# Kernel optimization log

Measured on AMD Instinct MI355X. Metric: run time of the kernel, lower is better.

The kernel has to match this reference:

```python
import jax, jax.numpy as jnp
import numpy as np

H = 8              # n_heads
N_PER_GRAPH = 64   # nodes per graph (equal-sized graphs)


def setup_inputs() -> dict:
    key = jax.random.key(0)
    ks = jax.random.split(key, 5)
    total, D = 65536, 512
    x = jax.random.normal(ks[0], (total, D), dtype=jnp.float32)
    batch = jnp.arange(total, dtype=jnp.int64) // N_PER_GRAPH  # sorted graph ids
    s = 1.0 / np.sqrt(D).astype(np.float32)
    # nn.MultiheadAttention packed in-proj (xavier-ish uniform) + zero bias
    in_proj_w = jax.random.uniform(ks[1], (3 * D, D), jnp.float32, -s, s)
    in_proj_b = jnp.zeros((3 * D,), jnp.float32)
    out_proj_w = jax.random.uniform(ks[2], (D, D), jnp.float32, -s, s)
    out_proj_b = jnp.zeros((D,), jnp.float32)
    gate_w = jax.random.uniform(ks[3], (1, D), jnp.float32, -s, s)
    gate_b = jnp.zeros((1,), jnp.float32)
    return {"x": x, "batch": batch, "in_proj_w": in_proj_w, "in_proj_b": in_proj_b,
            "out_proj_w": out_proj_w, "out_proj_b": out_proj_b,
            "gate_w": gate_w, "gate_b": gate_b}


def reference(x, batch, in_proj_w, in_proj_b, out_proj_w, out_proj_b, gate_w, gate_b):
    total, D = x.shape
    G = total // N_PER_GRAPH
    hd = D // H
    xg = x.reshape(G, N_PER_GRAPH, D)                       # [G, N, D]
    # packed qkv projection (torch: x @ in_proj_w.T + in_proj_b)
    qkv = jnp.einsum('gnd,ed->gne', xg, in_proj_w) + in_proj_b
    q, k, v = jnp.split(qkv, 3, axis=-1)
    def to_heads(t):
        return t.reshape(G, N_PER_GRAPH, H, hd).transpose(0, 2, 1, 3)  # [G, H, N, hd]
    q, k, v = to_heads(q), to_heads(k), to_heads(v)
    scores = jnp.einsum('ghnd,ghmd->ghnm', q, k) * (1.0 / np.sqrt(hd))
    attn = jax.nn.softmax(scores, axis=-1)
    ctx = jnp.einsum('ghnm,ghmd->ghnd', attn, v)
    ctx = ctx.transpose(0, 2, 1, 3).reshape(G, N_PER_GRAPH, D)
    attn_out = jnp.einsum('gnd,ed->gne', ctx, out_proj_w) + out_proj_b  # [G, N, D]
    gates = jax.nn.sigmoid(jnp.einsum('gnd,od->gno', attn_out, gate_w) + gate_b)
    return (attn_out * gates).sum(axis=1)                   # [G, D]
```

## Files before the change

kernel.cpp:

```cpp
#include <hip/hip_runtime.h>
#include <stdint.h>


typedef __attribute__((ext_vector_type(8))) short short8;
typedef __attribute__((ext_vector_type(4))) float f32x4;

#define D_ 512

#define WQKV_OFF   0u
#define WO_OFF     1572864u
#define UPART_OFF  2097152u
#define SG_OFF     2132032u
#define WCTX_OFF   2136128u
#define SCR_OFF    3184704u

__device__ __forceinline__ unsigned short f2bf(float f) {
    union { float f; unsigned int u; } t; t.f = f;
    unsigned int u = t.u;
    return (unsigned short)((u + 0x7FFFu + ((u >> 16) & 1u)) >> 16);
}
__device__ __forceinline__ unsigned pack2(float a, float b) {
    return (unsigned)f2bf(a) | ((unsigned)f2bf(b) << 16);
}

__global__ __launch_bounds__(256)
void convert_weights(const float* __restrict__ wqkv, const float* __restrict__ wo,
                     unsigned short* __restrict__ wbf,
                     const float* __restrict__ gw, float* __restrict__ upart) {
    if (blockIdx.x >= 1024) {
        const int b = blockIdx.x - 1024;
        const int t = threadIdx.x;
        float a0 = 0.f, a1 = 0.f;
        #pragma unroll 4
        for (int e = b * 32; e < b * 32 + 32; ++e) {
            const float ge = gw[e];
            a0 += wo[(size_t)e * 512 + t]       * ge;
            a1 += wo[(size_t)e * 512 + t + 256] * ge;
        }
        upart[b * 512 + t] = a0; upart[b * 512 + t + 256] = a1;
        return;
    }
    const int i4 = blockIdx.x * 256 + threadIdx.x;
    float4 v;
    if (i4 < 196608) v = *(const float4*)(wqkv + (size_t)i4 * 4);
    else             v = *(const float4*)(wo   + (size_t)(i4 - 196608) * 4);
    uint2 p; p.x = pack2(v.x, v.y); p.y = pack2(v.z, v.w);
    *(uint2*)(wbf + (size_t)i4 * 4) = p;
}

union U8 { unsigned u[4]; short8 s; };

__global__ __launch_bounds__(512, 2)
void attn_ctx_gscr(const float* __restrict__ x,
                   const unsigned short* __restrict__ wqkv,
                   const float* __restrict__ bqkv,
                   const float* __restrict__ upart,
                   const float* __restrict__ bo,
                   const float* __restrict__ gw,
                   const float* __restrict__ gb,
                   unsigned short* __restrict__ scr_g,
                   unsigned short* __restrict__ wctx_ws,
                   float* __restrict__ sumgate)
{
    __shared__ unsigned short xs[64][520];
    __shared__ float logitp[8][64];
    __shared__ float gatev[64];
    __shared__ float u_s[512];
    __shared__ float c0_s;

    const int g    = blockIdx.x;
    const int tid  = threadIdx.x;
    const int w    = tid >> 6;
    const int lane = tid & 63;
    const int l15  = lane & 15;
    const int quad = lane >> 4;

    #pragma unroll
    for (int i = 0; i < 16; ++i) {
        int idx = tid + i * 512;
        int row = idx >> 7;
        int c4  = idx & 127;
        float4 v = *(const float4*)(x + ((size_t)(g*64 + row))*512 + c4*4);
        uint2 p; p.x = pack2(v.x, v.y); p.y = pack2(v.z, v.w);
        *(uint2*)(&xs[row][c4*4]) = p;
    }
    {
        float s = 0.f;
        #pragma unroll
        for (int b = 0; b < 16; ++b) s += upart[b*512 + tid];
        u_s[tid] = s;
    }
    if (tid < 64) {
        float s = 0.f;
        #pragma unroll
        for (int i = 0; i < 8; ++i) s += bo[tid*8 + i] * gw[tid*8 + i];
        s += __shfl_xor(s, 1);  s += __shfl_xor(s, 2);  s += __shfl_xor(s, 4);
        s += __shfl_xor(s, 8);  s += __shfl_xor(s, 16); s += __shfl_xor(s, 32);
        if (tid == 0) c0_s = s + gb[0];
    }
    __syncthreads();

    const int h = w;
    unsigned short* Sg = scr_g + ((size_t)(g*8 + w) << 12);

    U8 qA[4][2], kB[4][2];
    #pragma unroll
    for (int dt = 0; dt < 4; ++dt) {
        f32x4 aq[4], ak[4], av[4];
        #pragma unroll
        for (int nt = 0; nt < 4; ++nt) {
            aq[nt] = (f32x4){0.f,0.f,0.f,0.f};
            ak[nt] = (f32x4){0.f,0.f,0.f,0.f};
            av[nt] = (f32x4){0.f,0.f,0.f,0.f};
        }
        const unsigned short* wq = wqkv + (size_t)(          h*64 + dt*16 + l15) * 512;
        const unsigned short* wk = wqkv + (size_t)( 512 +    h*64 + dt*16 + l15) * 512;
        const unsigned short* wv = wqkv + (size_t)(1024 +    h*64 + dt*16 + l15) * 512;
        #pragma unroll 4
        for (int ks = 0; ks < 16; ++ks) {
            const int col = ks*32 + quad*8;
            short8 a0 = *(const short8*)(wq + col);
            short8 a1 = *(const short8*)(wk + col);
            short8 a2 = *(const short8*)(wv + col);
            #pragma unroll
            for (int nt = 0; nt < 4; ++nt) {
                short8 b = *(const short8*)(&xs[nt*16 + l15][col]);
                aq[nt] = __builtin_amdgcn_mfma_f32_16x16x32_bf16(a0, b, aq[nt], 0,0,0);
                ak[nt] = __builtin_amdgcn_mfma_f32_16x16x32_bf16(a1, b, ak[nt], 0,0,0);
                av[nt] = __builtin_amdgcn_mfma_f32_16x16x32_bf16(a2, b, av[nt], 0,0,0);
            }
        }
        float bq[4], bk2[4], bv2[4];
        #pragma unroll
        for (int r = 0; r < 4; ++r) {
            bq[r]  = bqkv[          h*64 + dt*16 + quad*4 + r];
            bk2[r] = bqkv[ 512 +    h*64 + dt*16 + quad*4 + r];
            bv2[r] = bqkv[1024 +    h*64 + dt*16 + quad*4 + r];
        }
        const bool take = ((quad >> 1) == (dt & 1));
        const int  ks2  = dt >> 1;
        #pragma unroll
        for (int nt = 0; nt < 4; ++nt) {
            unsigned q01 = pack2(aq[nt][0]+bq[0],  aq[nt][1]+bq[1]);
            unsigned q23 = pack2(aq[nt][2]+bq[2],  aq[nt][3]+bq[3]);
            unsigned k01 = pack2(ak[nt][0]+bk2[0], ak[nt][1]+bk2[1]);
            unsigned k23 = pack2(ak[nt][2]+bk2[2], ak[nt][3]+bk2[3]);
            #pragma unroll
            for (int j = 0; j < 4; ++j) {
                int srcl = ((quad & 1)*2 + (j >> 1))*16 + l15;
                unsigned tq = (unsigned)__shfl((int)((j & 1) ? q23 : q01), srcl);
                unsigned tk = (unsigned)__shfl((int)((j & 1) ? k23 : k01), srcl);
                if (take) { qA[nt][ks2].u[j] = tq; kB[nt][ks2].u[j] = tk; }
            }
            #pragma unroll
            for (int r = 0; r < 4; ++r)
                Sg[(dt*16 + quad*4 + r)*64 + nt*16 + l15] = f2bf(av[nt][r] + bv2[r]);
        }
    }

    f32x4 sacc[4][4];
    #pragma unroll
    for (int a = 0; a < 4; ++a)
        #pragma unroll
        for (int b = 0; b < 4; ++b) sacc[a][b] = (f32x4){0.f,0.f,0.f,0.f};
    #pragma unroll
    for (int ks2 = 0; ks2 < 2; ++ks2)
        #pragma unroll
        for (int a = 0; a < 4; ++a)
            #pragma unroll
            for (int b = 0; b < 4; ++b)
                sacc[a][b] = __builtin_amdgcn_mfma_f32_16x16x32_bf16(
                                 qA[a][ks2].s, kB[b][ks2].s, sacc[a][b], 0,0,0);

    #pragma unroll
    for (int a = 0; a < 4; ++a) {
        #pragma unroll
        for (int r = 0; r < 4; ++r) {
            float m0 = -1e30f;
            #pragma unroll
            for (int b = 0; b < 4; ++b) { sacc[a][b][r] *= 0.125f; m0 = fmaxf(m0, sacc[a][b][r]); }
            m0 = fmaxf(m0, __shfl_xor(m0, 1));
            m0 = fmaxf(m0, __shfl_xor(m0, 2));
            m0 = fmaxf(m0, __shfl_xor(m0, 4));
            m0 = fmaxf(m0, __shfl_xor(m0, 8));
            float s = 0.f;
            #pragma unroll
            for (int b = 0; b < 4; ++b) { float e = __expf(sacc[a][b][r] - m0); sacc[a][b][r] = e; s += e; }
            s += __shfl_xor(s, 1); s += __shfl_xor(s, 2); s += __shfl_xor(s, 4); s += __shfl_xor(s, 8);
            float inv = 1.0f / s;
            #pragma unroll
            for (int b = 0; b < 4; ++b) sacc[a][b][r] *= inv;
        }
    }

    U8 vA[4][2];
    #pragma unroll
    for (int dtile = 0; dtile < 4; ++dtile)
        #pragma unroll
        for (int ks2 = 0; ks2 < 2; ++ks2)
            vA[dtile][ks2].s = *(const short8*)(Sg + (dtile*16 + l15)*64 + ks2*32 + quad*8);
    asm volatile("s_waitcnt vmcnt(0)" ::: "memory");

    #pragma unroll
    for (int a = 0; a < 4; ++a)
        #pragma unroll
        for (int b = 0; b < 4; ++b)
            #pragma unroll
            for (int r = 0; r < 4; ++r)
                Sg[(a*16 + quad*4 + r)*64 + b*16 + l15] = f2bf(sacc[a][b][r]);
    asm volatile("s_waitcnt vmcnt(0)" ::: "memory");

    U8 pB[4][2];
    #pragma unroll
    for (int a = 0; a < 4; ++a)
        #pragma unroll
        for (int ks2 = 0; ks2 < 2; ++ks2)
            pB[a][ks2].s = *(const short8*)(Sg + (a*16 + l15)*64 + ks2*32 + quad*8);

    f32x4 cacc[4][4];
    #pragma unroll
    for (int dtile = 0; dtile < 4; ++dtile)
        #pragma unroll
        for (int a = 0; a < 4; ++a) cacc[dtile][a] = (f32x4){0.f,0.f,0.f,0.f};
    #pragma unroll
    for (int ks2 = 0; ks2 < 2; ++ks2)
        #pragma unroll
        for (int dtile = 0; dtile < 4; ++dtile)
            #pragma unroll
            for (int a = 0; a < 4; ++a)
                cacc[dtile][a] = __builtin_amdgcn_mfma_f32_16x16x32_bf16(
                                     vA[dtile][ks2].s, pB[a][ks2].s, cacc[dtile][a], 0,0,0);

    {
        float uv[4][4];
        #pragma unroll
        for (int dtile = 0; dtile < 4; ++dtile)
            #pragma unroll
            for (int r = 0; r < 4; ++r)
                uv[dtile][r] = u_s[h*64 + dtile*16 + quad*4 + r];
        #pragma unroll
        for (int a = 0; a < 4; ++a) {
            float s = 0.f;
            #pragma unroll
            for (int dtile = 0; dtile < 4; ++dtile)
                #pragma unroll
                for (int r = 0; r < 4; ++r)
                    s += cacc[dtile][a][r] * uv[dtile][r];
            s += __shfl_xor(s, 16); s += __shfl_xor(s, 32);
            if (quad == 0) logitp[w][a*16 + l15] = s;
        }
    }
    __syncthreads();

    if (tid < 64) {
        float lg = c0_s;
        #pragma unroll
        for (int ww = 0; ww < 8; ++ww) lg += logitp[ww][tid];
        float gt = 1.0f / (1.0f + __expf(-lg));
        gatev[tid] = gt;
        float s = gt;
        s += __shfl_xor(s, 1);  s += __shfl_xor(s, 2);  s += __shfl_xor(s, 4);
        s += __shfl_xor(s, 8);  s += __shfl_xor(s, 16); s += __shfl_xor(s, 32);
        if (tid == 0) sumgate[g] = s;
    }
    __syncthreads();

    {
        float gv[4];
        #pragma unroll
        for (int a = 0; a < 4; ++a) gv[a] = gatev[a*16 + l15];
        #pragma unroll
        for (int dtile = 0; dtile < 4; ++dtile) {
            float sr[4];
            #pragma unroll
            for (int r = 0; r < 4; ++r) {
                float s = cacc[dtile][0][r]*gv[0] + cacc[dtile][1][r]*gv[1]
                        + cacc[dtile][2][r]*gv[2] + cacc[dtile][3][r]*gv[3];
                s += __shfl_xor(s, 1); s += __shfl_xor(s, 2);
                s += __shfl_xor(s, 4); s += __shfl_xor(s, 8);
                sr[r] = s;
            }
            if (l15 == 0) {
                uint2 pk; pk.x = pack2(sr[0], sr[1]); pk.y = pack2(sr[2], sr[3]);
                *(uint2*)(wctx_ws + (size_t)g*512 + h*64 + dtile*16 + quad*4) = pk;
            }
        }
    }
}

__global__ __launch_bounds__(512, 2)
void attn_ctx_lds(const float* __restrict__ x,
                  const unsigned short* __restrict__ wqkv,
                  const float* __restrict__ bqkv,
                  const float* __restrict__ upart,
                  const float* __restrict__ bo,
                  const float* __restrict__ gw,
                  const float* __restrict__ gb,
                  unsigned short* __restrict__ wctx_ws,
                  float* __restrict__ sumgate)
{
    __shared__ unsigned short xs[64][520];
    __shared__ unsigned short scr[8][64][72];
    __shared__ float logitp[8][64];
    __shared__ float gatev[64];
    __shared__ float u_s[512];
    __shared__ float c0_s;

    const int g    = blockIdx.x;
    const int tid  = threadIdx.x;
    const int w    = tid >> 6;
    const int lane = tid & 63;
    const int l15  = lane & 15;
    const int quad = lane >> 4;

    #pragma unroll
    for (int i = 0; i < 16; ++i) {
        int idx = tid + i * 512;
        int row = idx >> 7;
        int c4  = idx & 127;
        float4 v = *(const float4*)(x + ((size_t)(g*64 + row))*512 + c4*4);
        uint2 p; p.x = pack2(v.x, v.y); p.y = pack2(v.z, v.w);
        *(uint2*)(&xs[row][c4*4]) = p;
    }
    {
        float s = 0.f;
        #pragma unroll
        for (int b = 0; b < 16; ++b) s += upart[b*512 + tid];
        u_s[tid] = s;
    }
    if (tid < 64) {
        float s = 0.f;
        #pragma unroll
        for (int i = 0; i < 8; ++i) s += bo[tid*8 + i] * gw[tid*8 + i];
        s += __shfl_xor(s, 1);  s += __shfl_xor(s, 2);  s += __shfl_xor(s, 4);
        s += __shfl_xor(s, 8);  s += __shfl_xor(s, 16); s += __shfl_xor(s, 32);
        if (tid == 0) c0_s = s + gb[0];
    }
    __syncthreads();

    const int h = w;
    unsigned short (*S)[72] = scr[w];

    U8 qA[4][2], kB[4][2];
    #pragma unroll
    for (int dt = 0; dt < 4; ++dt) {
        f32x4 aq[4], ak[4], av[4];
        #pragma unroll
        for (int nt = 0; nt < 4; ++nt) {
            aq[nt] = (f32x4){0.f,0.f,0.f,0.f};
            ak[nt] = (f32x4){0.f,0.f,0.f,0.f};
            av[nt] = (f32x4){0.f,0.f,0.f,0.f};
        }
        const unsigned short* wq = wqkv + (size_t)(          h*64 + dt*16 + l15) * 512;
        const unsigned short* wk = wqkv + (size_t)( 512 +    h*64 + dt*16 + l15) * 512;
        const unsigned short* wv = wqkv + (size_t)(1024 +    h*64 + dt*16 + l15) * 512;
        #pragma unroll 4
        for (int ks = 0; ks < 16; ++ks) {
            const int col = ks*32 + quad*8;
            short8 a0 = *(const short8*)(wq + col);
            short8 a1 = *(const short8*)(wk + col);
            short8 a2 = *(const short8*)(wv + col);
            #pragma unroll
            for (int nt = 0; nt < 4; ++nt) {
                short8 b = *(const short8*)(&xs[nt*16 + l15][col]);
                aq[nt] = __builtin_amdgcn_mfma_f32_16x16x32_bf16(a0, b, aq[nt], 0,0,0);
                ak[nt] = __builtin_amdgcn_mfma_f32_16x16x32_bf16(a1, b, ak[nt], 0,0,0);
                av[nt] = __builtin_amdgcn_mfma_f32_16x16x32_bf16(a2, b, av[nt], 0,0,0);
            }
        }
        float bq[4], bk2[4], bv2[4];
        #pragma unroll
        for (int r = 0; r < 4; ++r) {
            bq[r]  = bqkv[          h*64 + dt*16 + quad*4 + r];
            bk2[r] = bqkv[ 512 +    h*64 + dt*16 + quad*4 + r];
            bv2[r] = bqkv[1024 +    h*64 + dt*16 + quad*4 + r];
        }
        const bool take = ((quad >> 1) == (dt & 1));
        const int  ks2  = dt >> 1;
        #pragma unroll
        for (int nt = 0; nt < 4; ++nt) {
            unsigned q01 = pack2(aq[nt][0]+bq[0],  aq[nt][1]+bq[1]);
            unsigned q23 = pack2(aq[nt][2]+bq[2],  aq[nt][3]+bq[3]);
            unsigned k01 = pack2(ak[nt][0]+bk2[0], ak[nt][1]+bk2[1]);
            unsigned k23 = pack2(ak[nt][2]+bk2[2], ak[nt][3]+bk2[3]);
            #pragma unroll
            for (int j = 0; j < 4; ++j) {
                int srcl = ((quad & 1)*2 + (j >> 1))*16 + l15;
                unsigned tq = (unsigned)__shfl((int)((j & 1) ? q23 : q01), srcl);
                unsigned tk = (unsigned)__shfl((int)((j & 1) ? k23 : k01), srcl);
                if (take) { qA[nt][ks2].u[j] = tq; kB[nt][ks2].u[j] = tk; }
            }
            #pragma unroll
            for (int r = 0; r < 4; ++r)
                S[dt*16 + quad*4 + r][nt*16 + l15] = f2bf(av[nt][r] + bv2[r]);
        }
    }

    f32x4 sacc[4][4];
    #pragma unroll
    for (int a = 0; a < 4; ++a)
        #pragma unroll
        for (int b = 0; b < 4; ++b) sacc[a][b] = (f32x4){0.f,0.f,0.f,0.f};
    #pragma unroll
    for (int ks2 = 0; ks2 < 2; ++ks2)
        #pragma unroll
        for (int a = 0; a < 4; ++a)
            #pragma unroll
            for (int b = 0; b < 4; ++b)
                sacc[a][b] = __builtin_amdgcn_mfma_f32_16x16x32_bf16(
                                 qA[a][ks2].s, kB[b][ks2].s, sacc[a][b], 0,0,0);

    #pragma unroll
    for (int a = 0; a < 4; ++a) {
        #pragma unroll
        for (int r = 0; r < 4; ++r) {
            float m0 = -1e30f;
            #pragma unroll
            for (int b = 0; b < 4; ++b) { sacc[a][b][r] *= 0.125f; m0 = fmaxf(m0, sacc[a][b][r]); }
            m0 = fmaxf(m0, __shfl_xor(m0, 1));
            m0 = fmaxf(m0, __shfl_xor(m0, 2));
            m0 = fmaxf(m0, __shfl_xor(m0, 4));
            m0 = fmaxf(m0, __shfl_xor(m0, 8));
            float s = 0.f;
            #pragma unroll
            for (int b = 0; b < 4; ++b) { float e = __expf(sacc[a][b][r] - m0); sacc[a][b][r] = e; s += e; }
            s += __shfl_xor(s, 1); s += __shfl_xor(s, 2); s += __shfl_xor(s, 4); s += __shfl_xor(s, 8);
            float inv = 1.0f / s;
            #pragma unroll
            for (int b = 0; b < 4; ++b) sacc[a][b][r] *= inv;
        }
    }

    U8 vA[4][2];
    #pragma unroll
    for (int dtile = 0; dtile < 4; ++dtile)
        #pragma unroll
        for (int ks2 = 0; ks2 < 2; ++ks2)
            vA[dtile][ks2].s = *(const short8*)(&S[dtile*16 + l15][ks2*32 + quad*8]);

    #pragma unroll
    for (int a = 0; a < 4; ++a)
        #pragma unroll
        for (int b = 0; b < 4; ++b)
            #pragma unroll
            for (int r = 0; r < 4; ++r)
                S[a*16 + quad*4 + r][b*16 + l15] = f2bf(sacc[a][b][r]);

    U8 pB[4][2];
    #pragma unroll
    for (int a = 0; a < 4; ++a)
        #pragma unroll
        for (int ks2 = 0; ks2 < 2; ++ks2)
            pB[a][ks2].s = *(const short8*)(&S[a*16 + l15][ks2*32 + quad*8]);

    f32x4 cacc[4][4];
    #pragma unroll
    for (int dtile = 0; dtile < 4; ++dtile)
        #pragma unroll
        for (int a = 0; a < 4; ++a) cacc[dtile][a] = (f32x4){0.f,0.f,0.f,0.f};
    #pragma unroll
    for (int ks2 = 0; ks2 < 2; ++ks2)
        #pragma unroll
        for (int dtile = 0; dtile < 4; ++dtile)
            #pragma unroll
            for (int a = 0; a < 4; ++a)
                cacc[dtile][a] = __builtin_amdgcn_mfma_f32_16x16x32_bf16(
                                     vA[dtile][ks2].s, pB[a][ks2].s, cacc[dtile][a], 0,0,0);

    {
        float uv[4][4];
        #pragma unroll
        for (int dtile = 0; dtile < 4; ++dtile)
            #pragma unroll
            for (int r = 0; r < 4; ++r)
                uv[dtile][r] = u_s[h*64 + dtile*16 + quad*4 + r];
        #pragma unroll
        for (int a = 0; a < 4; ++a) {
            float s = 0.f;
            #pragma unroll
            for (int dtile = 0; dtile < 4; ++dtile)
                #pragma unroll
                for (int r = 0; r < 4; ++r)
                    s += cacc[dtile][a][r] * uv[dtile][r];
            s += __shfl_xor(s, 16); s += __shfl_xor(s, 32);
            if (quad == 0) logitp[w][a*16 + l15] = s;
        }
    }
    __syncthreads();

    if (tid < 64) {
        float lg = c0_s;
        #pragma unroll
        for (int ww = 0; ww < 8; ++ww) lg += logitp[ww][tid];
        float gt = 1.0f / (1.0f + __expf(-lg));
        gatev[tid] = gt;
        float s = gt;
        s += __shfl_xor(s, 1);  s += __shfl_xor(s, 2);  s += __shfl_xor(s, 4);
        s += __shfl_xor(s, 8);  s += __shfl_xor(s, 16); s += __shfl_xor(s, 32);
        if (tid == 0) sumgate[g] = s;
    }
    __syncthreads();

    {
        float gv[4];
        #pragma unroll
        for (int a = 0; a < 4; ++a) gv[a] = gatev[a*16 + l15];
        #pragma unroll
        for (int dtile = 0; dtile < 4; ++dtile) {
            float sr[4];
            #pragma unroll
            for (int r = 0; r < 4; ++r) {
                float s = cacc[dtile][0][r]*gv[0] + cacc[dtile][1][r]*gv[1]
                        + cacc[dtile][2][r]*gv[2] + cacc[dtile][3][r]*gv[3];
                s += __shfl_xor(s, 1); s += __shfl_xor(s, 2);
                s += __shfl_xor(s, 4); s += __shfl_xor(s, 8);
                sr[r] = s;
            }
            if (l15 == 0) {
                uint2 pk; pk.x = pack2(sr[0], sr[1]); pk.y = pack2(sr[2], sr[3]);
                *(uint2*)(wctx_ws + (size_t)g*512 + h*64 + dtile*16 + quad*4) = pk;
            }
        }
    }
}

__global__ __launch_bounds__(256, 4)
void outproj_kernel(const unsigned short* __restrict__ wo_bf,
                    const unsigned short* __restrict__ wctx_bf,
                    const float* __restrict__ bo,
                    const float* __restrict__ sumgate,
                    float* __restrict__ out)
{
    const int tid  = threadIdx.x;
    const int w    = tid >> 6;
    const int lane = tid & 63;
    const int l15  = lane & 15;
    const int quad = lane >> 4;
    const int g0   = blockIdx.x * 16;
    const int e0   = blockIdx.y * 64;

    f32x4 oac = (f32x4){0.f,0.f,0.f,0.f};
    #pragma unroll 4
    for (int ks = 0; ks < 16; ++ks) {
        const int col = ks*32 + quad*8;
        short8 a = *(const short8*)(wctx_bf + (size_t)(g0 + l15)*D_ + col);
        short8 b = *(const short8*)(wo_bf + (size_t)(e0 + w*16 + l15)*D_ + col);
        oac = __builtin_amdgcn_mfma_f32_16x16x32_bf16(a, b, oac, 0,0,0);
    }
    const int e = e0 + w*16 + l15;
    const float bov = bo[e];
    #pragma unroll
    for (int r = 0; r < 4; ++r) {
        const int gg = g0 + quad*4 + r;
        out[(size_t)gg*D_ + e] = oac[r] + sumgate[gg] * bov;
    }
}

extern "C" void kernel_launch(void* const* d_in, const int* in_sizes, int n_in,
                              void* d_out, int out_size, void* d_ws, size_t ws_size,
                              hipStream_t stream) {
    const float* x    = (const float*)d_in[0];
    const float* wqkv = (const float*)d_in[2];
    const float* bqkv = (const float*)d_in[3];
    const float* wo   = (const float*)d_in[4];
    const float* bo   = (const float*)d_in[5];
    const float* gw   = (const float*)d_in[6];
    const float* gb   = (const float*)d_in[7];
    float* out = (float*)d_out;

    char* ws = (char*)d_ws;
    unsigned short* wqkv_bf = (unsigned short*)(ws + WQKV_OFF);
    unsigned short* wo_bf   = (unsigned short*)(ws + WO_OFF);
    float*          upart   = (float*)(ws + UPART_OFF);
    float*          sg_ws   = (float*)(ws + SG_OFF);
    unsigned short* wctx_ws = (unsigned short*)(ws + WCTX_OFF);
    unsigned short* scr_g   = (unsigned short*)(ws + SCR_OFF);

    const int total = in_sizes[0] / D_;
    const int G     = total / 64;

    const size_t need_fast = (size_t)SCR_OFF + (size_t)G * 8 * 8192;
    const bool   fast      = ws_size >= need_fast;

    hipLaunchKernelGGL(convert_weights, dim3(1040), dim3(256), 0, stream,
                       wqkv, wo, wqkv_bf, gw, upart);
    if (fast) {
        hipLaunchKernelGGL(attn_ctx_gscr, dim3(G), dim3(512), 0, stream,
                           x, wqkv_bf, bqkv, upart, bo, gw, gb, scr_g, wctx_ws, sg_ws);
    } else {
        hipLaunchKernelGGL(attn_ctx_lds, dim3(G), dim3(512), 0, stream,
                           x, wqkv_bf, bqkv, upart, bo, gw, gb, wctx_ws, sg_ws);
    }
    hipLaunchKernelGGL(outproj_kernel, dim3(G/16, 8), dim3(256), 0, stream,
                       wo_bf, wctx_ws, bo, sg_ws, out);
}
```

Before: 434.6 us.

## Fuse weight conversion, attention, and out-projection into one cooperative persistent kernel

Replaces the three-kernel pipeline with a single cooperative kernel of 256 persistent blocks. Grid-wide syncs separate three phases: weight conversion to bf16, per-graph attention with a loop over graphs, and the output projection. The global-memory scratch path for V and P is dropped in favour of LDS scratch. The aim is to remove launch gaps and global scratch traffic. In exchange, only 256 blocks run with low occupancy, work per block is serialized, and a launch fallback is kept.

```diff
diff --git a/kernel.cpp b/kernel.cpp
--- a/kernel.cpp
+++ b/kernel.cpp
@@ -1,6 +1,9 @@
 #include <hip/hip_runtime.h>
+#include <hip/hip_cooperative_groups.h>
 #include <stdint.h>
 
+
+namespace cg = cooperative_groups;
 
 typedef __attribute__((ext_vector_type(8))) short short8;
 typedef __attribute__((ext_vector_type(4))) float f32x4;
@@ -12,7 +15,6 @@
 #define UPART_OFF  2097152u
 #define SG_OFF     2132032u
 #define WCTX_OFF   2136128u
-#define SCR_OFF    3184704u
 
 __device__ __forceinline__ unsigned short f2bf(float f) {
     union { float f; unsigned int u; } t; t.f = f;
@@ -21,6 +23,296 @@
 }
 __device__ __forceinline__ unsigned pack2(float a, float b) {
     return (unsigned)f2bf(a) | ((unsigned)f2bf(b) << 16);
+}
+
+union U8 { unsigned u[4]; short8 s; };
+
+__global__ __launch_bounds__(512, 2)
+void fused_all(const float* __restrict__ x,
+               const float* __restrict__ wqkv_f,
+               const float* __restrict__ wo_f,
+               const float* __restrict__ bqkv,
+               const float* __restrict__ bo,
+               const float* __restrict__ gw,
+               const float* __restrict__ gb,
+               unsigned short* __restrict__ wbf,
+               float* __restrict__ upart,
+               unsigned short* __restrict__ wctx_ws,
+               float* __restrict__ sumgate,
+               float* __restrict__ out,
+               int G)
+{
+    __shared__ unsigned short xs[64][520];
+    __shared__ unsigned short scr[8][64][72];
+    __shared__ float logitp[8][64];
+    __shared__ float gatev[64];
+    __shared__ float u_s[512];
+    __shared__ float c0_s;
+
+    const int bid  = blockIdx.x;
+    const int tid  = threadIdx.x;
+    const int w    = tid >> 6;
+    const int lane = tid & 63;
+    const int l15  = lane & 15;
+    const int quad = lane >> 4;
+
+    for (int i4 = bid * 512 + tid; i4 < 262144; i4 += 256 * 512) {
+        float4 v;
+        if (i4 < 196608) v = *(const float4*)(wqkv_f + (size_t)i4 * 4);
+        else             v = *(const float4*)(wo_f   + (size_t)(i4 - 196608) * 4);
+        uint2 p; p.x = pack2(v.x, v.y); p.y = pack2(v.z, v.w);
+        *(uint2*)(wbf + (size_t)i4 * 4) = p;
+    }
+    if (bid < 16) {
+        float a = 0.f;
+        #pragma unroll 4
+        for (int e = bid * 32; e < bid * 32 + 32; ++e)
+            a += wo_f[(size_t)e * 512 + tid] * gw[e];
+        upart[bid * 512 + tid] = a;
+    }
+    cg::this_grid().sync();
+
+    const unsigned short* wqkv  = wbf;
+    const unsigned short* wo_bf = wbf + 786432;
+
+    {
+        float s = 0.f;
+        #pragma unroll
+        for (int b = 0; b < 16; ++b) s += upart[b*512 + tid];
+        u_s[tid] = s;
+    }
+    if (tid < 64) {
+        float s = 0.f;
+        #pragma unroll
+        for (int i = 0; i < 8; ++i) s += bo[tid*8 + i] * gw[tid*8 + i];
+        s += __shfl_xor(s, 1);  s += __shfl_xor(s, 2);  s += __shfl_xor(s, 4);
+        s += __shfl_xor(s, 8);  s += __shfl_xor(s, 16); s += __shfl_xor(s, 32);
+        if (tid == 0) c0_s = s + gb[0];
+    }
+    __syncthreads();
+
+    const int h = w;
+    unsigned short (*S)[72] = scr[w];
+
+    for (int g = bid; g < G; g += 256) {
+        #pragma unroll
+        for (int i = 0; i < 16; ++i) {
+            int idx = tid + i * 512;
+            int row = idx >> 7;
+            int c4  = idx & 127;
+            float4 v = *(const float4*)(x + ((size_t)(g*64 + row))*512 + c4*4);
+            uint2 p; p.x = pack2(v.x, v.y); p.y = pack2(v.z, v.w);
+            *(uint2*)(&xs[row][c4*4]) = p;
+        }
+        __syncthreads();
+
+        U8 qA[4][2], kB[4][2];
+        #pragma unroll
+        for (int dt = 0; dt < 4; ++dt) {
+            f32x4 aq[4], ak[4], av[4];
+            #pragma unroll
+            for (int nt = 0; nt < 4; ++nt) {
+                aq[nt] = (f32x4){0.f,0.f,0.f,0.f};
+                ak[nt] = (f32x4){0.f,0.f,0.f,0.f};
+                av[nt] = (f32x4){0.f,0.f,0.f,0.f};
+            }
+            const unsigned short* wq = wqkv + (size_t)(          h*64 + dt*16 + l15) * 512;
+            const unsigned short* wk = wqkv + (size_t)( 512 +    h*64 + dt*16 + l15) * 512;
+            const unsigned short* wv = wqkv + (size_t)(1024 +    h*64 + dt*16 + l15) * 512;
+            #pragma unroll 4
+            for (int ks = 0; ks < 16; ++ks) {
+                const int col = ks*32 + quad*8;
+                short8 a0 = *(const short8*)(wq + col);
+                short8 a1 = *(const short8*)(wk + col);
+                short8 a2 = *(const short8*)(wv + col);
+                #pragma unroll
+                for (int nt = 0; nt < 4; ++nt) {
+                    short8 b = *(const short8*)(&xs[nt*16 + l15][col]);
+                    aq[nt] = __builtin_amdgcn_mfma_f32_16x16x32_bf16(a0, b, aq[nt], 0,0,0);
+                    ak[nt] = __builtin_amdgcn_mfma_f32_16x16x32_bf16(a1, b, ak[nt], 0,0,0);
+                    av[nt] = __builtin_amdgcn_mfma_f32_16x16x32_bf16(a2, b, av[nt], 0,0,0);
+                }
+            }
+            float bq[4], bk2[4], bv2[4];
+            #pragma unroll
+            for (int r = 0; r < 4; ++r) {
+                bq[r]  = bqkv[          h*64 + dt*16 + quad*4 + r];
+                bk2[r] = bqkv[ 512 +    h*64 + dt*16 + quad*4 + r];
+                bv2[r] = bqkv[1024 +    h*64 + dt*16 + quad*4 + r];
+            }
+            const bool take = ((quad >> 1) == (dt & 1));
+            const int  ks2  = dt >> 1;
+            #pragma unroll
+            for (int nt = 0; nt < 4; ++nt) {
+                unsigned q01 = pack2(aq[nt][0]+bq[0],  aq[nt][1]+bq[1]);
+                unsigned q23 = pack2(aq[nt][2]+bq[2],  aq[nt][3]+bq[3]);
+                unsigned k01 = pack2(ak[nt][0]+bk2[0], ak[nt][1]+bk2[1]);
+                unsigned k23 = pack2(ak[nt][2]+bk2[2], ak[nt][3]+bk2[3]);
+                #pragma unroll
+                for (int j = 0; j < 4; ++j) {
+                    int srcl = ((quad & 1)*2 + (j >> 1))*16 + l15;
+                    unsigned tq = (unsigned)__shfl((int)((j & 1) ? q23 : q01), srcl);
+                    unsigned tk = (unsigned)__shfl((int)((j & 1) ? k23 : k01), srcl);
+                    if (take) { qA[nt][ks2].u[j] = tq; kB[nt][ks2].u[j] = tk; }
+                }
+                #pragma unroll
+                for (int r = 0; r < 4; ++r)
+                    S[dt*16 + quad*4 + r][nt*16 + l15] = f2bf(av[nt][r] + bv2[r]);
+            }
+        }
+
+        f32x4 sacc[4][4];
+        #pragma unroll
+        for (int a = 0; a < 4; ++a)
+            #pragma unroll
+            for (int b = 0; b < 4; ++b) sacc[a][b] = (f32x4){0.f,0.f,0.f,0.f};
+        #pragma unroll
+        for (int ks2 = 0; ks2 < 2; ++ks2)
+            #pragma unroll
+            for (int a = 0; a < 4; ++a)
+                #pragma unroll
+                for (int b = 0; b < 4; ++b)
+                    sacc[a][b] = __builtin_amdgcn_mfma_f32_16x16x32_bf16(
+                                     qA[a][ks2].s, kB[b][ks2].s, sacc[a][b], 0,0,0);
+
+        #pragma unroll
+        for (int a = 0; a < 4; ++a) {
+            #pragma unroll
+            for (int r = 0; r < 4; ++r) {
+                float m0 = -1e30f;
+                #pragma unroll
+                for (int b = 0; b < 4; ++b) { sacc[a][b][r] *= 0.125f; m0 = fmaxf(m0, sacc[a][b][r]); }
+                m0 = fmaxf(m0, __shfl_xor(m0, 1));
+                m0 = fmaxf(m0, __shfl_xor(m0, 2));
+                m0 = fmaxf(m0, __shfl_xor(m0, 4));
+                m0 = fmaxf(m0, __shfl_xor(m0, 8));
+                float s = 0.f;
+                #pragma unroll
+                for (int b = 0; b < 4; ++b) { float e = __expf(sacc[a][b][r] - m0); sacc[a][b][r] = e; s += e; }
+                s += __shfl_xor(s, 1); s += __shfl_xor(s, 2); s += __shfl_xor(s, 4); s += __shfl_xor(s, 8);
+                float inv = 1.0f / s;
+                #pragma unroll
+                for (int b = 0; b < 4; ++b) sacc[a][b][r] *= inv;
+            }
+        }
+
+        U8 vA[4][2];
+        #pragma unroll
+        for (int dtile = 0; dtile < 4; ++dtile)
+            #pragma unroll
+            for (int ks2 = 0; ks2 < 2; ++ks2)
+                vA[dtile][ks2].s = *(const short8*)(&S[dtile*16 + l15][ks2*32 + quad*8]);
+
+        #pragma unroll
+        for (int a = 0; a < 4; ++a)
+            #pragma unroll
+            for (int b = 0; b < 4; ++b)
+                #pragma unroll
+                for (int r = 0; r < 4; ++r)
+                    S[a*16 + quad*4 + r][b*16 + l15] = f2bf(sacc[a][b][r]);
+
+        U8 pB[4][2];
+        #pragma unroll
+        for (int a = 0; a < 4; ++a)
+            #pragma unroll
+            for (int ks2 = 0; ks2 < 2; ++ks2)
+                pB[a][ks2].s = *(const short8*)(&S[a*16 + l15][ks2*32 + quad*8]);
+
+        f32x4 cacc[4][4];
+        #pragma unroll
+        for (int dtile = 0; dtile < 4; ++dtile)
+            #pragma unroll
+            for (int a = 0; a < 4; ++a) cacc[dtile][a] = (f32x4){0.f,0.f,0.f,0.f};
+        #pragma unroll
+        for (int ks2 = 0; ks2 < 2; ++ks2)
+            #pragma unroll
+            for (int dtile = 0; dtile < 4; ++dtile)
+                #pragma unroll
+                for (int a = 0; a < 4; ++a)
+                    cacc[dtile][a] = __builtin_amdgcn_mfma_f32_16x16x32_bf16(
+                                         vA[dtile][ks2].s, pB[a][ks2].s, cacc[dtile][a], 0,0,0);
+
+        {
+            float uv[4][4];
+            #pragma unroll
+            for (int dtile = 0; dtile < 4; ++dtile)
+                #pragma unroll
+                for (int r = 0; r < 4; ++r)
+                    uv[dtile][r] = u_s[h*64 + dtile*16 + quad*4 + r];
+            #pragma unroll
+            for (int a = 0; a < 4; ++a) {
+                float s = 0.f;
+                #pragma unroll
+                for (int dtile = 0; dtile < 4; ++dtile)
+                    #pragma unroll
+                    for (int r = 0; r < 4; ++r)
+                        s += cacc[dtile][a][r] * uv[dtile][r];
+                s += __shfl_xor(s, 16); s += __shfl_xor(s, 32);
+                if (quad == 0) logitp[w][a*16 + l15] = s;
+            }
+        }
+        __syncthreads();
+
+        if (tid < 64) {
+            float lg = c0_s;
+            #pragma unroll
+            for (int ww = 0; ww < 8; ++ww) lg += logitp[ww][tid];
+            float gt = 1.0f / (1.0f + __expf(-lg));
+            gatev[tid] = gt;
+            float s = gt;
+            s += __shfl_xor(s, 1);  s += __shfl_xor(s, 2);  s += __shfl_xor(s, 4);
+            s += __shfl_xor(s, 8);  s += __shfl_xor(s, 16); s += __shfl_xor(s, 32);
+            if (tid == 0) sumgate[g] = s;
+        }
+        __syncthreads();
+
+        {
+            float gv[4];
+            #pragma unroll
+            for (int a = 0; a < 4; ++a) gv[a] = gatev[a*16 + l15];
+            #pragma unroll
+            for (int dtile = 0; dtile < 4; ++dtile) {
+                float sr[4];
+                #pragma unroll
+                for (int r = 0; r < 4; ++r) {
+                    float s = cacc[dtile][0][r]*gv[0] + cacc[dtile][1][r]*gv[1]
+                            + cacc[dtile][2][r]*gv[2] + cacc[dtile][3][r]*gv[3];
+                    s += __shfl_xor(s, 1); s += __shfl_xor(s, 2);
+                    s += __shfl_xor(s, 4); s += __shfl_xor(s, 8);
+                    sr[r] = s;
+                }
+                if (l15 == 0) {
+                    uint2 pk; pk.x = pack2(sr[0], sr[1]); pk.y = pack2(sr[2], sr[3]);
+                    *(uint2*)(wctx_ws + (size_t)g*512 + h*64 + dtile*16 + quad*4) = pk;
+                }
+            }
+        }
+        __syncthreads();
+    }
+
+    cg::this_grid().sync();
+
+    const int GX = G >> 4;
+    for (int job = bid; job < GX * 4; job += 256) {
+        const int gx = job % GX;
+        const int e0 = (job / GX) * 128;
+        const int g0 = gx * 16;
+        f32x4 oac = (f32x4){0.f,0.f,0.f,0.f};
+        #pragma unroll 4
+        for (int ks = 0; ks < 16; ++ks) {
+            const int col = ks*32 + quad*8;
+            short8 a = *(const short8*)(wctx_ws + (size_t)(g0 + l15)*D_ + col);
+            short8 b = *(const short8*)(wo_bf + (size_t)(e0 + w*16 + l15)*D_ + col);
+            oac = __builtin_amdgcn_mfma_f32_16x16x32_bf16(a, b, oac, 0,0,0);
+        }
+        const int e = e0 + w*16 + l15;
+        const float bov = bo[e];
+        #pragma unroll
+        for (int r = 0; r < 4; ++r) {
+            const int gg = g0 + quad*4 + r;
+            out[(size_t)gg*D_ + e] = oac[r] + sumgate[gg] * bov;
+        }
+    }
 }
 
 __global__ __launch_bounds__(256)
@@ -48,256 +340,16 @@
     *(uint2*)(wbf + (size_t)i4 * 4) = p;
 }
 
-union U8 { unsigned u[4]; short8 s; };
-
 __global__ __launch_bounds__(512, 2)
-void attn_ctx_gscr(const float* __restrict__ x,
-                   const unsigned short* __restrict__ wqkv,
-                   const float* __restrict__ bqkv,
-                   const float* __restrict__ upart,
-                   const float* __restrict__ bo,
-                   const float* __restrict__ gw,
-                   const float* __restrict__ gb,
-                   unsigned short* __restrict__ scr_g,
-                   unsigned short* __restrict__ wctx_ws,
-                   float* __restrict__ sumgate)
-{
-    __shared__ unsigned short xs[64][520];
-    __shared__ float logitp[8][64];
-    __shared__ float gatev[64];
-    __shared__ float u_s[512];
-    __shared__ float c0_s;
-
-    const int g    = blockIdx.x;
-    const int tid  = threadIdx.x;
-    const int w    = tid >> 6;
-    const int lane = tid & 63;
-    const int l15  = lane & 15;
-    const int quad = lane >> 4;
-
-    #pragma unroll
-    for (int i = 0; i < 16; ++i) {
-        int idx = tid + i * 512;
-        int row = idx >> 7;
-        int c4  = idx & 127;
-        float4 v = *(const float4*)(x + ((size_t)(g*64 + row))*512 + c4*4);
-        uint2 p; p.x = pack2(v.x, v.y); p.y = pack2(v.z, v.w);
-        *(uint2*)(&xs[row][c4*4]) = p;
-    }
-    {
-        float s = 0.f;
-        #pragma unroll
-        for (int b = 0; b < 16; ++b) s += upart[b*512 + tid];
-        u_s[tid] = s;
-    }
-    if (tid < 64) {
-        float s = 0.f;
-        #pragma unroll
-        for (int i = 0; i < 8; ++i) s += bo[tid*8 + i] * gw[tid*8 + i];
-        s += __shfl_xor(s, 1);  s += __shfl_xor(s, 2);  s += __shfl_xor(s, 4);
-        s += __shfl_xor(s, 8);  s += __shfl_xor(s, 16); s += __shfl_xor(s, 32);
-        if (tid == 0) c0_s = s + gb[0];
-    }
-    __syncthreads();
-
-    const int h = w;
-    unsigned short* Sg = scr_g + ((size_t)(g*8 + w) << 12);
-
-    U8 qA[4][2], kB[4][2];
-    #pragma unroll
-    for (int dt = 0; dt < 4; ++dt) {
-        f32x4 aq[4], ak[4], av[4];
-        #pragma unroll
-        for (int nt = 0; nt < 4; ++nt) {
-            aq[nt] = (f32x4){0.f,0.f,0.f,0.f};
-            ak[nt] = (f32x4){0.f,0.f,0.f,0.f};
-            av[nt] = (f32x4){0.f,0.f,0.f,0.f};
-        }
-        const unsigned short* wq = wqkv + (size_t)(          h*64 + dt*16 + l15) * 512;
-        const unsigned short* wk = wqkv + (size_t)( 512 +    h*64 + dt*16 + l15) * 512;
-        const unsigned short* wv = wqkv + (size_t)(1024 +    h*64 + dt*16 + l15) * 512;
-        #pragma unroll 4
-        for (int ks = 0; ks < 16; ++ks) {
-            const int col = ks*32 + quad*8;
-            short8 a0 = *(const short8*)(wq + col);
-            short8 a1 = *(const short8*)(wk + col);
-            short8 a2 = *(const short8*)(wv + col);
-            #pragma unroll
-            for (int nt = 0; nt < 4; ++nt) {
-                short8 b = *(const short8*)(&xs[nt*16 + l15][col]);
-                aq[nt] = __builtin_amdgcn_mfma_f32_16x16x32_bf16(a0, b, aq[nt], 0,0,0);
-                ak[nt] = __builtin_amdgcn_mfma_f32_16x16x32_bf16(a1, b, ak[nt], 0,0,0);
-                av[nt] = __builtin_amdgcn_mfma_f32_16x16x32_bf16(a2, b, av[nt], 0,0,0);
-            }
-        }
-        float bq[4], bk2[4], bv2[4];
-        #pragma unroll
-        for (int r = 0; r < 4; ++r) {
-            bq[r]  = bqkv[          h*64 + dt*16 + quad*4 + r];
-            bk2[r] = bqkv[ 512 +    h*64 + dt*16 + quad*4 + r];
-            bv2[r] = bqkv[1024 +    h*64 + dt*16 + quad*4 + r];
-        }
-        const bool take = ((quad >> 1) == (dt & 1));
-        const int  ks2  = dt >> 1;
-        #pragma unroll
-        for (int nt = 0; nt < 4; ++nt) {
-            unsigned q01 = pack2(aq[nt][0]+bq[0],  aq[nt][1]+bq[1]);
-            unsigned q23 = pack2(aq[nt][2]+bq[2],  aq[nt][3]+bq[3]);
-            unsigned k01 = pack2(ak[nt][0]+bk2[0], ak[nt][1]+bk2[1]);
-            unsigned k23 = pack2(ak[nt][2]+bk2[2], ak[nt][3]+bk2[3]);
-            #pragma unroll
-            for (int j = 0; j < 4; ++j) {
-                int srcl = ((quad & 1)*2 + (j >> 1))*16 + l15;
-                unsigned tq = (unsigned)__shfl((int)((j & 1) ? q23 : q01), srcl);
-                unsigned tk = (unsigned)__shfl((int)((j & 1) ? k23 : k01), srcl);
-                if (take) { qA[nt][ks2].u[j] = tq; kB[nt][ks2].u[j] = tk; }
-            }
-            #pragma unroll
-            for (int r = 0; r < 4; ++r)
-                Sg[(dt*16 + quad*4 + r)*64 + nt*16 + l15] = f2bf(av[nt][r] + bv2[r]);
-        }
-    }
-
-    f32x4 sacc[4][4];
-    #pragma unroll
-    for (int a = 0; a < 4; ++a)
-        #pragma unroll
-        for (int b = 0; b < 4; ++b) sacc[a][b] = (f32x4){0.f,0.f,0.f,0.f};
-    #pragma unroll
-    for (int ks2 = 0; ks2 < 2; ++ks2)
-        #pragma unroll
-        for (int a = 0; a < 4; ++a)
-            #pragma unroll
-            for (int b = 0; b < 4; ++b)
-                sacc[a][b] = __builtin_amdgcn_mfma_f32_16x16x32_bf16(
-                                 qA[a][ks2].s, kB[b][ks2].s, sacc[a][b], 0,0,0);
-
-    #pragma unroll
-    for (int a = 0; a < 4; ++a) {
-        #pragma unroll
-        for (int r = 0; r < 4; ++r) {
-            float m0 = -1e30f;
-            #pragma unroll
-            for (int b = 0; b < 4; ++b) { sacc[a][b][r] *= 0.125f; m0 = fmaxf(m0, sacc[a][b][r]); }
-            m0 = fmaxf(m0, __shfl_xor(m0, 1));
-            m0 = fmaxf(m0, __shfl_xor(m0, 2));
-            m0 = fmaxf(m0, __shfl_xor(m0, 4));
-            m0 = fmaxf(m0, __shfl_xor(m0, 8));
-            float s = 0.f;
-            #pragma unroll
-            for (int b = 0; b < 4; ++b) { float e = __expf(sacc[a][b][r] - m0); sacc[a][b][r] = e; s += e; }
-            s += __shfl_xor(s, 1); s += __shfl_xor(s, 2); s += __shfl_xor(s, 4); s += __shfl_xor(s, 8);
-            float inv = 1.0f / s;
-            #pragma unroll
-            for (int b = 0; b < 4; ++b) sacc[a][b][r] *= inv;
-        }
-    }
-
-    U8 vA[4][2];
-    #pragma unroll
-    for (int dtile = 0; dtile < 4; ++dtile)
-        #pragma unroll
-        for (int ks2 = 0; ks2 < 2; ++ks2)
-            vA[dtile][ks2].s = *(const short8*)(Sg + (dtile*16 + l15)*64 + ks2*32 + quad*8);
-    asm volatile("s_waitcnt vmcnt(0)" ::: "memory");
-
-    #pragma unroll
-    for (int a = 0; a < 4; ++a)
-        #pragma unroll
-        for (int b = 0; b < 4; ++b)
-            #pragma unroll
-            for (int r = 0; r < 4; ++r)
-                Sg[(a*16 + quad*4 + r)*64 + b*16 + l15] = f2bf(sacc[a][b][r]);
-    asm volatile("s_waitcnt vmcnt(0)" ::: "memory");
-
-    U8 pB[4][2];
-    #pragma unroll
-    for (int a = 0; a < 4; ++a)
-        #pragma unroll
-        for (int ks2 = 0; ks2 < 2; ++ks2)
-            pB[a][ks2].s = *(const short8*)(Sg + (a*16 + l15)*64 + ks2*32 + quad*8);
-
-    f32x4 cacc[4][4];
-    #pragma unroll
-    for (int dtile = 0; dtile < 4; ++dtile)
-        #pragma unroll
-        for (int a = 0; a < 4; ++a) cacc[dtile][a] = (f32x4){0.f,0.f,0.f,0.f};
-    #pragma unroll
-    for (int ks2 = 0; ks2 < 2; ++ks2)
-        #pragma unroll
-        for (int dtile = 0; dtile < 4; ++dtile)
-            #pragma unroll
-            for (int a = 0; a < 4; ++a)
-                cacc[dtile][a] = __builtin_amdgcn_mfma_f32_16x16x32_bf16(
-                                     vA[dtile][ks2].s, pB[a][ks2].s, cacc[dtile][a], 0,0,0);
-
-    {
-        float uv[4][4];
-        #pragma unroll
-        for (int dtile = 0; dtile < 4; ++dtile)
-            #pragma unroll
-            for (int r = 0; r < 4; ++r)
-                uv[dtile][r] = u_s[h*64 + dtile*16 + quad*4 + r];
-        #pragma unroll
-        for (int a = 0; a < 4; ++a) {
-            float s = 0.f;
-            #pragma unroll
-            for (int dtile = 0; dtile < 4; ++dtile)
-                #pragma unroll
-                for (int r = 0; r < 4; ++r)
-                    s += cacc[dtile][a][r] * uv[dtile][r];
-            s += __shfl_xor(s, 16); s += __shfl_xor(s, 32);
-            if (quad == 0) logitp[w][a*16 + l15] = s;
-        }
-    }
-    __syncthreads();
-
-    if (tid < 64) {
-        float lg = c0_s;
-        #pragma unroll
-        for (int ww = 0; ww < 8; ++ww) lg += logitp[ww][tid];
-        float gt = 1.0f / (1.0f + __expf(-lg));
-        gatev[tid] = gt;
-        float s = gt;
-        s += __shfl_xor(s, 1);  s += __shfl_xor(s, 2);  s += __shfl_xor(s, 4);
-        s += __shfl_xor(s, 8);  s += __shfl_xor(s, 16); s += __shfl_xor(s, 32);
-        if (tid == 0) sumgate[g] = s;
-    }
-    __syncthreads();
-
-    {
-        float gv[4];
-        #pragma unroll
-        for (int a = 0; a < 4; ++a) gv[a] = gatev[a*16 + l15];
-        #pragma unroll
-        for (int dtile = 0; dtile < 4; ++dtile) {
-            float sr[4];
-            #pragma unroll
-            for (int r = 0; r < 4; ++r) {
-                float s = cacc[dtile][0][r]*gv[0] + cacc[dtile][1][r]*gv[1]
-                        + cacc[dtile][2][r]*gv[2] + cacc[dtile][3][r]*gv[3];
-                s += __shfl_xor(s, 1); s += __shfl_xor(s, 2);
-                s += __shfl_xor(s, 4); s += __shfl_xor(s, 8);
-                sr[r] = s;
-            }
-            if (l15 == 0) {
-                uint2 pk; pk.x = pack2(sr[0], sr[1]); pk.y = pack2(sr[2], sr[3]);
-                *(uint2*)(wctx_ws + (size_t)g*512 + h*64 + dtile*16 + quad*4) = pk;
-            }
-        }
-    }
-}
-
-__global__ __launch_bounds__(512, 2)
-void attn_ctx_lds(const float* __restrict__ x,
-                  const unsigned short* __restrict__ wqkv,
-                  const float* __restrict__ bqkv,
-                  const float* __restrict__ upart,
-                  const float* __restrict__ bo,
-                  const float* __restrict__ gw,
-                  const float* __restrict__ gb,
-                  unsigned short* __restrict__ wctx_ws,
-                  float* __restrict__ sumgate)
+void attn_ctx_kernel(const float* __restrict__ x,
+                     const unsigned short* __restrict__ wqkv,
+                     const float* __restrict__ bqkv,
+                     const float* __restrict__ upart,
+                     const float* __restrict__ bo,
+                     const float* __restrict__ gw,
+                     const float* __restrict__ gb,
+                     unsigned short* __restrict__ wctx_ws,
+                     float* __restrict__ sumgate)
 {
     __shared__ unsigned short xs[64][520];
     __shared__ unsigned short scr[8][64][72];
@@ -569,28 +621,29 @@
     float* out = (float*)d_out;
 
     char* ws = (char*)d_ws;
-    unsigned short* wqkv_bf = (unsigned short*)(ws + WQKV_OFF);
+    unsigned short* wbf     = (unsigned short*)(ws + WQKV_OFF);
     unsigned short* wo_bf   = (unsigned short*)(ws + WO_OFF);
     float*          upart   = (float*)(ws + UPART_OFF);
     float*          sg_ws   = (float*)(ws + SG_OFF);
     unsigned short* wctx_ws = (unsigned short*)(ws + WCTX_OFF);
-    unsigned short* scr_g   = (unsigned short*)(ws + SCR_OFF);
 
     const int total = in_sizes[0] / D_;
-    const int G     = total / 64;
-
-    const size_t need_fast = (size_t)SCR_OFF + (size_t)G * 8 * 8192;
-    const bool   fast      = ws_size >= need_fast;
+    int G = total / 64;
+
+    void* args[] = { (void*)&x, (void*)&wqkv, (void*)&wo, (void*)&bqkv,
+                     (void*)&bo, (void*)&gw, (void*)&gb, (void*)&wbf,
+                     (void*)&upart, (void*)&wctx_ws, (void*)&sg_ws,
+                     (void*)&out, (void*)&G };
+    hipError_t err = hipLaunchCooperativeKernel((const void*)fused_all,
+                                                dim3(256), dim3(512),
+                                                args, 0, stream);
+    if (err == hipSuccess) return;
+    (void)hipGetLastError();
 
     hipLaunchKernelGGL(convert_weights, dim3(1040), dim3(256), 0, stream,
-                       wqkv, wo, wqkv_bf, gw, upart);
-    if (fast) {
-        hipLaunchKernelGGL(attn_ctx_gscr, dim3(G), dim3(512), 0, stream,
-                           x, wqkv_bf, bqkv, upart, bo, gw, gb, scr_g, wctx_ws, sg_ws);
-    } else {
-        hipLaunchKernelGGL(attn_ctx_lds, dim3(G), dim3(512), 0, stream,
-                           x, wqkv_bf, bqkv, upart, bo, gw, gb, wctx_ws, sg_ws);
-    }
+                       wqkv, wo, wbf, gw, upart);
+    hipLaunchKernelGGL(attn_ctx_kernel, dim3(G), dim3(512), 0, stream,
+                       x, wbf, bqkv, upart, bo, gw, gb, wctx_ws, sg_ws);
     hipLaunchKernelGGL(outproj_kernel, dim3(G/16, 8), dim3(256), 0, stream,
                        wo_bf, wctx_ws, bo, sg_ws, out);
 }
```

After: 584.1 us. 34.4% more time.
